# Kernel optimization log

Hardware: AMD Instinct MI355X
Metric: run time of the kernel (lower is better)

The kernel has to match this reference:

```python
import jax, jax.numpy as jnp
import numpy as np

N_NODES, N_EDGES, EMB_DIM = 100000, 1000000, 64
NUM_BOND_TYPE, NUM_BOND_DIR = 6, 3  # self-loop bond type index = 4


def gcn_conv(x, src, dst, bond_type, bond_dir, W, b, emb_bond, emb_dir):
    """One GCNConv (Hu et al. mol-GNN variant). src/dst/attrs already include self-loops."""
    N = x.shape[0]
    edge_emb = emb_bond[bond_type] + emb_dir[bond_dir]           # [Etot, D]
    ones = jnp.ones(src.shape[0], x.dtype)
    deg = jax.ops.segment_sum(ones, src, num_segments=N)         # scatter_add over row
    dis = jnp.where(deg > 0, jax.lax.rsqrt(deg), 0.0)
    norm = dis[src] * dis[dst]                                   # [Etot]
    h = x @ W.T + b                                              # [N, D]
    msg = norm[:, None] * (h[src] + edge_emb)                    # [Etot, D]
    return jax.ops.segment_sum(msg, dst, num_segments=N)         # add-aggregate at target


def with_self_loops(edge_index, edge_attr, N):
    loop = jnp.arange(N, dtype=edge_index.dtype)
    src = jnp.concatenate([edge_index[0], loop])
    dst = jnp.concatenate([edge_index[1], loop])
    bt = jnp.concatenate([edge_attr[:, 0], jnp.full((N,), 4, edge_attr.dtype)])
    bd = jnp.concatenate([edge_attr[:, 1], jnp.zeros((N,), edge_attr.dtype)])
    return src, dst, bt, bd


def setup_inputs() -> dict:
    key = jax.random.key(0)
    ks = jax.random.split(key, 12)
    D = EMB_DIM
    s = 1.0 / np.sqrt(D)
    inp = {
        "x": jax.random.normal(ks[0], (N_NODES, D), jnp.float32),
        "edge_index": jax.random.randint(ks[1], (2, N_EDGES), 0, N_NODES, jnp.int64 if jax.config.jax_enable_x64 else jnp.int32),
        "edge_attr": jax.random.randint(ks[2], (N_EDGES, 2), 0, 3, jnp.int64 if jax.config.jax_enable_x64 else jnp.int32),
        "W1": jax.random.uniform(ks[3], (D, D), jnp.float32, -s, s),
        "b1": jax.random.uniform(ks[4], (D,), jnp.float32, -s, s),
        "ebond1": jax.random.normal(ks[5], (NUM_BOND_TYPE, D), jnp.float32) * 0.1,
        "edir1": jax.random.normal(ks[6], (NUM_BOND_DIR, D), jnp.float32) * 0.1,
        "W2": jax.random.uniform(ks[7], (D, D), jnp.float32, -s, s),
        "b2": jax.random.uniform(ks[8], (D,), jnp.float32, -s, s),
        "ebond2": jax.random.normal(ks[9], (NUM_BOND_TYPE, D), jnp.float32) * 0.1,
        "edir2": jax.random.normal(ks[10], (NUM_BOND_DIR, D), jnp.float32) * 0.1,
    }
    return inp


def reference(x, edge_index, edge_attr, W1, b1, ebond1, edir1, W2, b2, ebond2, edir2):
    N = x.shape[0]
    src, dst, bt, bd = with_self_loops(edge_index, edge_attr, N)
    h = gcn_conv(x, src, dst, bt, bd, W1, b1, ebond1, edir1)
    h = jax.nn.relu(h)
    out = gcn_conv(h, src, dst, bt, bd, W2, b2, ebond2, edir2)
    return out
```

## Files before the change

### kernel.cpp

```cpp
#include <hip/hip_runtime.h>


#define THREADS 256
#define NBINS 512
#define BCAP 4096
#define CHUNK 2048
#define GEMM_SMEM_BYTES (64 * 68 * 4)
#define SC_SMEM (CHUNK * 4 * 2 + CHUNK * 2 * 2 + 6 * NBINS * 4 + 256 * 4)

typedef __attribute__((ext_vector_type(8))) short bf16x8;
typedef __attribute__((ext_vector_type(4))) float f32x4;

__device__ __forceinline__ float bflo(unsigned int v) { return __uint_as_float(v << 16); }
__device__ __forceinline__ float bfhi(unsigned int v) { return __uint_as_float(v & 0xFFFF0000u); }
__device__ __forceinline__ unsigned short f2bf(float f) {
    unsigned int u = __float_as_uint(f);
    return (unsigned short)((u + 0x7FFFu + ((u >> 16) & 1u)) >> 16);
}
__device__ __forceinline__ int sb(unsigned int w, int j) {
    return (int)(w << (24 - 8 * j)) >> 24;
}

template <bool XBF16>
__device__ __forceinline__ void gemm64_body(int tile, const void* __restrict__ Xv,
                                            const float* __restrict__ W,
                                            const float* __restrict__ B,
                                            unsigned short* __restrict__ Hb,
                                            unsigned char* __restrict__ Hq,
                                            float2* __restrict__ dsc, int N,
                                            float (*smem)[68]) {
    int t = threadIdx.x;
    int lane = t & 63;
    int wave = __builtin_amdgcn_readfirstlane(t >> 6);
    int l15 = lane & 15;
    int lk = lane >> 4;
    int arow = tile * 64 + wave * 16 + l15;

    bf16x8 a0, a1;
    if (arow < N) {
        if (XBF16) {
            const unsigned short* xp = (const unsigned short*)Xv + (size_t)arow * 64 + 8 * lk;
            a0 = *(const bf16x8*)xp;
            a1 = *(const bf16x8*)(xp + 32);
        } else {
            const float* xp = (const float*)Xv + (size_t)arow * 64 + 8 * lk;
            float4 v0 = *(const float4*)xp;
            float4 v1 = *(const float4*)(xp + 4);
            float4 v2 = *(const float4*)(xp + 32);
            float4 v3 = *(const float4*)(xp + 36);
            a0[0] = (short)f2bf(v0.x); a0[1] = (short)f2bf(v0.y);
            a0[2] = (short)f2bf(v0.z); a0[3] = (short)f2bf(v0.w);
            a0[4] = (short)f2bf(v1.x); a0[5] = (short)f2bf(v1.y);
            a0[6] = (short)f2bf(v1.z); a0[7] = (short)f2bf(v1.w);
            a1[0] = (short)f2bf(v2.x); a1[1] = (short)f2bf(v2.y);
            a1[2] = (short)f2bf(v2.z); a1[3] = (short)f2bf(v2.w);
            a1[4] = (short)f2bf(v3.x); a1[5] = (short)f2bf(v3.y);
            a1[6] = (short)f2bf(v3.z); a1[7] = (short)f2bf(v3.w);
        }
    } else {
#pragma unroll
        for (int e = 0; e < 8; ++e) { a0[e] = 0; a1[e] = 0; }
    }

    bf16x8 bfr[4][2];
#pragma unroll
    for (int n = 0; n < 4; ++n) {
        const float* wp = W + (size_t)(16 * n + l15) * 64 + 8 * lk;
#pragma unroll
        for (int ks = 0; ks < 2; ++ks) {
            float4 u0 = *(const float4*)(wp + 32 * ks);
            float4 u1 = *(const float4*)(wp + 32 * ks + 4);
            bf16x8 bb;
            bb[0] = (short)f2bf(u0.x); bb[1] = (short)f2bf(u0.y);
            bb[2] = (short)f2bf(u0.z); bb[3] = (short)f2bf(u0.w);
            bb[4] = (short)f2bf(u1.x); bb[5] = (short)f2bf(u1.y);
            bb[6] = (short)f2bf(u1.z); bb[7] = (short)f2bf(u1.w);
            bfr[n][ks] = bb;
        }
    }

    f32x4 acc[4];
#pragma unroll
    for (int n = 0; n < 4; ++n) {
        f32x4 z = {0.0f, 0.0f, 0.0f, 0.0f};
        z = __builtin_amdgcn_mfma_f32_16x16x32_bf16(a0, bfr[n][0], z, 0, 0, 0);
        acc[n] = __builtin_amdgcn_mfma_f32_16x16x32_bf16(a1, bfr[n][1], z, 0, 0, 0);
    }

#pragma unroll
    for (int n = 0; n < 4; ++n) {
        float bv = B[16 * n + l15];
        int col = 16 * n + l15;
#pragma unroll
        for (int r = 0; r < 4; ++r)
            smem[16 * wave + 4 * lk + r][col] = acc[n][r] + bv;
    }
    __syncthreads();

#pragma unroll
    for (int i = 0; i < 2; ++i) {
        int idx = t + i * THREADS;
        int r = idx >> 3;
        int c8 = (idx & 7) << 3;
        int grow = tile * 64 + r;
        float4 va = *(const float4*)(&smem[r][c8]);
        float4 vb = *(const float4*)(&smem[r][c8 + 4]);
        float v[8] = {va.x, va.y, va.z, va.w, vb.x, vb.y, vb.z, vb.w};
        float m = fabsf(v[0]);
#pragma unroll
        for (int j = 1; j < 8; ++j) m = fmaxf(m, fabsf(v[j]));
        m = fmaxf(m, __shfl_xor(m, 1));
        m = fmaxf(m, __shfl_xor(m, 2));
        m = fmaxf(m, __shfl_xor(m, 4));
        if (grow < N) {
            uint4 o;
            o.x = (unsigned)f2bf(v[0]) | ((unsigned)f2bf(v[1]) << 16);
            o.y = (unsigned)f2bf(v[2]) | ((unsigned)f2bf(v[3]) << 16);
            o.z = (unsigned)f2bf(v[4]) | ((unsigned)f2bf(v[5]) << 16);
            o.w = (unsigned)f2bf(v[6]) | ((unsigned)f2bf(v[7]) << 16);
            *(uint4*)(Hb + (size_t)grow * 64 + c8) = o;
            float inv = m > 0.0f ? 127.0f / m : 0.0f;
            int q[8];
#pragma unroll
            for (int j = 0; j < 8; ++j) q[j] = __float2int_rn(v[j] * inv);
            uint2 qp;
            qp.x = (unsigned)(q[0] & 255) | ((unsigned)(q[1] & 255) << 8) |
                   ((unsigned)(q[2] & 255) << 16) | ((unsigned)(q[3] & 255) << 24);
            qp.y = (unsigned)(q[4] & 255) | ((unsigned)(q[5] & 255) << 8) |
                   ((unsigned)(q[6] & 255) << 16) | ((unsigned)(q[7] & 255) << 24);
            *(uint2*)(Hq + (size_t)grow * 64 + c8) = qp;
            if ((idx & 7) == 0) dsc[grow].y = m * (1.0f / 127.0f);
        }
    }
}

__global__ __launch_bounds__(THREADS) void zero_gemm_kernel(
    int* __restrict__ gcur, int ncur, const float* __restrict__ X,
    const float* __restrict__ W1, const float* __restrict__ B1,
    unsigned short* __restrict__ Hb, unsigned char* __restrict__ Hq,
    float2* __restrict__ dsc, int N, int tile0) {
    __shared__ __align__(16) char sh[GEMM_SMEM_BYTES];
    int b = blockIdx.x;
    if (b == 0) {
        for (int i = threadIdx.x; i < ncur; i += THREADS) gcur[i] = 0;
        return;
    }
    gemm64_body<false>(tile0 + b - 1, X, W1, B1, Hb, Hq, dsc, N, (float(*)[68])sh);
}

__global__ __launch_bounds__(THREADS) void scatter_kernel(
    const int* __restrict__ src, const int* __restrict__ dst, const int* __restrict__ attr,
    int* __restrict__ gcurS, int* __restrict__ gcurD, unsigned char* __restrict__ payS,
    unsigned int* __restrict__ payD, int E, int SCB,
    const float* __restrict__ X, const float* __restrict__ W1, const float* __restrict__ B1,
    unsigned short* __restrict__ Hb, unsigned char* __restrict__ Hq,
    float2* __restrict__ dsc, int N, int tile0) {
    __shared__ __align__(16) char sh[SC_SMEM];
    int b = blockIdx.x;
    if (b >= SCB) {
        gemm64_body<false>(tile0 + b - SCB, X, W1, B1, Hb, Hq, dsc, N, (float(*)[68])sh);
        return;
    }
    unsigned int* Wv = (unsigned int*)sh;
    unsigned int* SD = Wv + CHUNK;
    unsigned short* DB = (unsigned short*)(SD + CHUNK);
    unsigned short* SDB = DB + CHUNK;
    int* hD = (int*)(SDB + CHUNK);
    int* hS = hD + NBINS;
    int* mapD = hS + NBINS;
    int* mapS = mapD + NBINS;
    int* curD = mapS + NBINS;
    int* curS = curD + NBINS;
    int* scn = curS + NBINS;
    unsigned char* SS = (unsigned char*)Wv;
    unsigned short* SSB = DB;

    int t = threadIdx.x;
    for (int k = t; k < NBINS; k += THREADS) { hD[k] = 0; hS[k] = 0; }
    __syncthreads();

    int lo = b * CHUNK, hi = min(E, lo + CHUNK);
    int nch = hi - lo;
    const int2* ap = (const int2*)attr;
    for (int li = t; li < nch; li += THREADS) {
        int i = lo + li;
        int sv = src[i], dv = dst[i];
        int2 a = ap[i];
        Wv[li] = (unsigned int)sv | ((unsigned int)(a.x * 3 + a.y) << 17) |
                 ((unsigned int)(dv & 255) << 22);
        DB[li] = (unsigned short)(dv >> 8);
        atomicAdd(&hD[dv >> 8], 1);
        atomicAdd(&hS[sv >> 8], 1);
    }
    __syncthreads();

    for (int k = t; k < NBINS; k += THREADS) {
        int h = hD[k];
        int r = h ? atomicAdd(&gcurD[k], h) : 0;
        mapD[k] = k * BCAP + r;
        int h2 = hS[k];
        int r2 = h2 ? atomicAdd(&gcurS[k], h2) : 0;
        mapS[k] = k * BCAP + r2;
    }
    __syncthreads();

    scn[t] = hD[2 * t] + hD[2 * t + 1];
    __syncthreads();
    for (int d = 1; d < THREADS; d <<= 1) {
        int a = (t >= d) ? scn[t - d] : 0;
        __syncthreads();
        scn[t] += a;
        __syncthreads();
    }
    {
        int off = t ? scn[t - 1] : 0;
        curD[2 * t] = off;
        curD[2 * t + 1] = off + hD[2 * t];
        mapD[2 * t] -= off;
        mapD[2 * t + 1] -= off + hD[2 * t];
    }
    __syncthreads();
    scn[t] = hS[2 * t] + hS[2 * t + 1];
    __syncthreads();
    for (int d = 1; d < THREADS; d <<= 1) {
        int a = (t >= d) ? scn[t - d] : 0;
        __syncthreads();
        scn[t] += a;
        __syncthreads();
    }
    {
        int off = t ? scn[t - 1] : 0;
        curS[2 * t] = off;
        curS[2 * t + 1] = off + hS[2 * t];
        mapS[2 * t] -= off;
        mapS[2 * t + 1] -= off + hS[2 * t];
    }
    __syncthreads();

    for (int li = t; li < nch; li += THREADS) {
        int k = DB[li];
        int p = atomicAdd(&curD[k], 1);
        SD[p] = Wv[li];
        SDB[p] = (unsigned short)k;
    }
    __syncthreads();

    for (int li = t; li < nch; li += THREADS) {
        int val = (int)(SD[li] & 0x1FFFFu);
        int k = val >> 8;
        int p = atomicAdd(&curS[k], 1);
        SS[p] = (unsigned char)(val & 255);
        SSB[p] = (unsigned short)k;
    }
    __syncthreads();

    for (int li = t; li < nch; li += THREADS) {
        payD[mapD[SDB[li]] + li] = SD[li];
        payS[mapS[SSB[li]] + li] = SS[li];
    }
}

__global__ __launch_bounds__(THREADS) void build_kernel(
    const unsigned char* __restrict__ payS, const unsigned int* __restrict__ payD,
    const int* __restrict__ gcurS, const int* __restrict__ gcurD,
    unsigned int* __restrict__ sorted, int2* __restrict__ rc,
    int NB2, float2* __restrict__ dsc, int N) {
    __shared__ int cnt[256];
    __shared__ int cur[256];
    __shared__ int s[THREADS];
    int t = threadIdx.x;
    int b = blockIdx.x;
    if (b < NB2) {
        int k = b;
        cnt[t] = 0;
        __syncthreads();
        int n = gcurS[k], off = k * BCAP;
        for (int i = t; i < n; i += THREADS) atomicAdd(&cnt[payS[off + i]], 1);
        __syncthreads();
        int node = k * 256 + t;
        if (node < N) dsc[node].x = 1.0f / sqrtf(1.0f + (float)cnt[t]);
    } else {
        int k = b - NB2;
        cnt[t] = 0;
        __syncthreads();
        int ecnt = gcurD[k], eoff = k * BCAP;
        for (int i = t; i < ecnt; i += THREADS)
            atomicAdd(&cnt[(payD[eoff + i] >> 22) & 255], 1);
        __syncthreads();
        int v = cnt[t];
        s[t] = v;
        __syncthreads();
        for (int d = 1; d < THREADS; d <<= 1) {
            int a = (t >= d) ? s[t - d] : 0;
            __syncthreads();
            s[t] += a;
            __syncthreads();
        }
        int excl = s[t] - v;
        int node = k * 256 + t;
        if (node < N) rc[node] = make_int2(eoff + excl, v);
        cur[t] = excl;
        __syncthreads();
        for (int i = t; i < ecnt; i += THREADS) {
            unsigned int u = payD[eoff + i];
            int p = atomicAdd(&cur[(u >> 22) & 255], 1);
            sorted[eoff + p] = u & 0x3FFFFFu;
        }
    }
}

template <bool XBF16>
__global__ __launch_bounds__(THREADS) void gemm64_kernel(const void* __restrict__ Xv,
                                                         const float* __restrict__ W,
                                                         const float* __restrict__ B,
                                                         unsigned short* __restrict__ Hb,
                                                         unsigned char* __restrict__ Hq,
                                                         float2* __restrict__ dsc, int N) {
    __shared__ __align__(16) char sh[GEMM_SMEM_BYTES];
    gemm64_body<XBF16>(blockIdx.x, Xv, W, B, Hb, Hq, dsc, N, (float(*)[68])sh);
}

__device__ __forceinline__ void edge_acc(unsigned int u, float dn,
                                         const float2* __restrict__ dsc,
                                         const unsigned char* __restrict__ Hq, int c,
                                         const float (*embc)[64], float acc[8]) {
    int s0 = u & 0x1FFFF;
    int e0 = (u >> 17) & 31;
    float2 ds = dsc[s0];
    uint2 q = *(const uint2*)(Hq + (size_t)s0 * 64 + c);
    float w = ds.x * dn, ws = w * ds.y;
    float4 ea = *(const float4*)(&embc[e0][c]);
    float4 eb = *(const float4*)(&embc[e0][c + 4]);
    acc[0] = fmaf(ws, (float)sb(q.x, 0), fmaf(w, ea.x, acc[0]));
    acc[1] = fmaf(ws, (float)sb(q.x, 1), fmaf(w, ea.y, acc[1]));
    acc[2] = fmaf(ws, (float)sb(q.x, 2), fmaf(w, ea.z, acc[2]));
    acc[3] = fmaf(ws, (float)sb(q.x, 3), fmaf(w, ea.w, acc[3]));
    acc[4] = fmaf(ws, (float)sb(q.y, 0), fmaf(w, eb.x, acc[4]));
    acc[5] = fmaf(ws, (float)sb(q.y, 1), fmaf(w, eb.y, acc[5]));
    acc[6] = fmaf(ws, (float)sb(q.y, 2), fmaf(w, eb.z, acc[6]));
    acc[7] = fmaf(ws, (float)sb(q.y, 3), fmaf(w, eb.w, acc[7]));
}

template <bool RELU_BF16_OUT>
__global__ __launch_bounds__(THREADS) void aggregate_kernel(
    const unsigned short* __restrict__ Hb, const unsigned char* __restrict__ Hq,
    const float2* __restrict__ dsc, const float* __restrict__ ebond,
    const float* __restrict__ edir, const int2* __restrict__ rc,
    const unsigned int* __restrict__ entries, void* __restrict__ outv, int N) {
    __shared__ float embc[18][64];
    int t = threadIdx.x;
    for (int i = t; i < 18 * 64; i += THREADS) {
        int row = i >> 6, c = i & 63;
        embc[row][c] = ebond[(row / 3) * 64 + c] + edir[(row % 3) * 64 + c];
    }
    __syncthreads();

    int n = blockIdx.x * 32 + (t >> 3);
    if (n >= N) return;
    int c = (t & 7) << 3;

    float dn = dsc[n].x;
    uint4 hv = *(const uint4*)(Hb + (size_t)n * 64 + c);
    float4 ea = *(const float4*)(&embc[12][c]);
    float4 eb = *(const float4*)(&embc[12][c + 4]);
    float nrm = dn * dn;
    float accA[8], accB[8];
    accA[0] = nrm * (bflo(hv.x) + ea.x);
    accA[1] = nrm * (bfhi(hv.x) + ea.y);
    accA[2] = nrm * (bflo(hv.y) + ea.z);
    accA[3] = nrm * (bfhi(hv.y) + ea.w);
    accA[4] = nrm * (bflo(hv.z) + eb.x);
    accA[5] = nrm * (bfhi(hv.z) + eb.y);
    accA[6] = nrm * (bflo(hv.w) + eb.z);
    accA[7] = nrm * (bfhi(hv.w) + eb.w);
#pragma unroll
    for (int j = 0; j < 8; ++j) accB[j] = 0.0f;

    int2 pc = rc[n];
    int p = pc.x;
    int end = p + pc.y;
    const float(*ec)[64] = (const float(*)[64])embc;
    for (; p + 3 < end; p += 4) {
        unsigned int u0 = entries[p];
        unsigned int u1 = entries[p + 1];
        unsigned int u2 = entries[p + 2];
        unsigned int u3 = entries[p + 3];
        edge_acc(u0, dn, dsc, Hq, c, ec, accA);
        edge_acc(u1, dn, dsc, Hq, c, ec, accB);
        edge_acc(u2, dn, dsc, Hq, c, ec, accA);
        edge_acc(u3, dn, dsc, Hq, c, ec, accB);
    }
    for (; p < end; ++p) edge_acc(entries[p], dn, dsc, Hq, c, ec, accA);

    float o[8];
#pragma unroll
    for (int j = 0; j < 8; ++j) o[j] = accA[j] + accB[j];

    if (RELU_BF16_OUT) {
        unsigned short* ob = (unsigned short*)outv;
        uint4 ov;
        ov.x = (unsigned)f2bf(fmaxf(o[0], 0.0f)) | ((unsigned)f2bf(fmaxf(o[1], 0.0f)) << 16);
        ov.y = (unsigned)f2bf(fmaxf(o[2], 0.0f)) | ((unsigned)f2bf(fmaxf(o[3], 0.0f)) << 16);
        ov.z = (unsigned)f2bf(fmaxf(o[4], 0.0f)) | ((unsigned)f2bf(fmaxf(o[5], 0.0f)) << 16);
        ov.w = (unsigned)f2bf(fmaxf(o[6], 0.0f)) | ((unsigned)f2bf(fmaxf(o[7], 0.0f)) << 16);
        *(uint4*)(ob + (size_t)n * 64 + c) = ov;
    } else {
        float* of = (float*)outv;
        *(float4*)(of + (size_t)n * 64 + c) = make_float4(o[0], o[1], o[2], o[3]);
        *(float4*)(of + (size_t)n * 64 + c + 4) = make_float4(o[4], o[5], o[6], o[7]);
    }
}

extern "C" void kernel_launch(void* const* d_in, const int* in_sizes, int n_in,
                              void* d_out, int out_size, void* d_ws, size_t ws_size,
                              hipStream_t stream) {
    const float* x      = (const float*)d_in[0];
    const int*   eidx   = (const int*)d_in[1];
    const int*   eattr  = (const int*)d_in[2];
    const float* W1     = (const float*)d_in[3];
    const float* b1     = (const float*)d_in[4];
    const float* ebond1 = (const float*)d_in[5];
    const float* edir1  = (const float*)d_in[6];
    const float* W2     = (const float*)d_in[7];
    const float* b2     = (const float*)d_in[8];
    const float* ebond2 = (const float*)d_in[9];
    const float* edir2  = (const float*)d_in[10];

    const int N = in_sizes[0] / 64;
    const int E = in_sizes[1] / 2;
    const int* src = eidx;
    const int* dst = eidx + E;
    float* out = (float*)d_out;
    const int NB2 = (N + 255) >> 8;
    const int SCB = (E + CHUNK - 1) / CHUNK;

    char* w = (char*)d_ws;
    size_t Na = ((size_t)N * 4 + 255) & ~(size_t)255;
    float2* dsc    = (float2*)w;           w += 2 * Na;
    int2*  rc      = (int2*)w;             w += 2 * Na;
    int*   gcur    = (int*)w;              w += 2 * NBINS * 4;
    unsigned int* payD   = (unsigned int*)w;   w += (size_t)NBINS * BCAP * 4;
    unsigned int* sorted = (unsigned int*)w;   w += (size_t)NBINS * BCAP * 4;
    unsigned char* payS  = (unsigned char*)w;  w += (size_t)NBINS * BCAP;
    unsigned short* Hb   = (unsigned short*)w; w += (size_t)N * 64 * 2;
    unsigned char*  Hq   = (unsigned char*)w;  w += ((size_t)N * 64 + 255) & ~(size_t)255;
    unsigned short* Ab   = (unsigned short*)w; w += (size_t)N * 64 * 2;
    int* gcurS = gcur;
    int* gcurD = gcur + NBINS;

    const int gT   = (N + 63) / 64;
    const int gN32 = (N + 31) / 32;

    const int t0 = min(gT, 512);
    const int t1 = gT - t0;

    zero_gemm_kernel<<<1 + t0, THREADS, 0, stream>>>(gcur, 2 * NBINS, x, W1, b1, Hb, Hq,
                                                     dsc, N, 0);
    scatter_kernel<<<SCB + t1, THREADS, 0, stream>>>(src, dst, eattr, gcurS, gcurD, payS,
                                                     payD, E, SCB, x, W1, b1, Hb, Hq,
                                                     dsc, N, t0);
    build_kernel<<<2 * NB2, THREADS, 0, stream>>>(payS, payD, gcurS, gcurD, sorted,
                                                  rc, NB2, dsc, N);

    aggregate_kernel<true><<<gN32, THREADS, 0, stream>>>(Hb, Hq, dsc, ebond1, edir1, rc,
                                                         sorted, Ab, N);

    gemm64_kernel<true><<<gT, THREADS, 0, stream>>>(Ab, W2, b2, Hb, Hq, dsc, N);
    aggregate_kernel<false><<<gN32, THREADS, 0, stream>>>(Hb, Hq, dsc, ebond2, edir2, rc,
                                                          sorted, out, N);
}
```

Before: 220.7 us.

## Fuse layer-1 aggregation with layer-2 GEMM in one kernel

Merges the first aggregation and the second linear layer into one kernel. Each block aggregates 64 nodes into shared memory as bf16, then runs the MFMA GEMM and writes the bf16/int8 features for layer 2. This drops one launch and the round trip of the intermediate activation through global memory. Because the GEMM overwrote the features layer 1 was still reading, it now writes to double buffers (Hb2/Hq2/dsc2). The trade-off is larger blocks with more shared memory and fewer threads in flight per node during aggregation.

```diff
diff --git a/kernel.cpp b/kernel.cpp
--- a/kernel.cpp
+++ b/kernel.cpp
@@ -21,48 +21,8 @@
     return (int)(w << (24 - 8 * j)) >> 24;
 }
 
-template <bool XBF16>
-__device__ __forceinline__ void gemm64_body(int tile, const void* __restrict__ Xv,
-                                            const float* __restrict__ W,
-                                            const float* __restrict__ B,
-                                            unsigned short* __restrict__ Hb,
-                                            unsigned char* __restrict__ Hq,
-                                            float2* __restrict__ dsc, int N,
-                                            float (*smem)[68]) {
-    int t = threadIdx.x;
-    int lane = t & 63;
-    int wave = __builtin_amdgcn_readfirstlane(t >> 6);
-    int l15 = lane & 15;
-    int lk = lane >> 4;
-    int arow = tile * 64 + wave * 16 + l15;
-
-    bf16x8 a0, a1;
-    if (arow < N) {
-        if (XBF16) {
-            const unsigned short* xp = (const unsigned short*)Xv + (size_t)arow * 64 + 8 * lk;
-            a0 = *(const bf16x8*)xp;
-            a1 = *(const bf16x8*)(xp + 32);
-        } else {
-            const float* xp = (const float*)Xv + (size_t)arow * 64 + 8 * lk;
-            float4 v0 = *(const float4*)xp;
-            float4 v1 = *(const float4*)(xp + 4);
-            float4 v2 = *(const float4*)(xp + 32);
-            float4 v3 = *(const float4*)(xp + 36);
-            a0[0] = (short)f2bf(v0.x); a0[1] = (short)f2bf(v0.y);
-            a0[2] = (short)f2bf(v0.z); a0[3] = (short)f2bf(v0.w);
-            a0[4] = (short)f2bf(v1.x); a0[5] = (short)f2bf(v1.y);
-            a0[6] = (short)f2bf(v1.z); a0[7] = (short)f2bf(v1.w);
-            a1[0] = (short)f2bf(v2.x); a1[1] = (short)f2bf(v2.y);
-            a1[2] = (short)f2bf(v2.z); a1[3] = (short)f2bf(v2.w);
-            a1[4] = (short)f2bf(v3.x); a1[5] = (short)f2bf(v3.y);
-            a1[6] = (short)f2bf(v3.z); a1[7] = (short)f2bf(v3.w);
-        }
-    } else {
-#pragma unroll
-        for (int e = 0; e < 8; ++e) { a0[e] = 0; a1[e] = 0; }
-    }
-
-    bf16x8 bfr[4][2];
+__device__ __forceinline__ void load_bfrags(const float* __restrict__ W, int l15, int lk,
+                                            bf16x8 bfr[4][2]) {
 #pragma unroll
     for (int n = 0; n < 4; ++n) {
         const float* wp = W + (size_t)(16 * n + l15) * 64 + 8 * lk;
@@ -78,15 +38,17 @@
             bfr[n][ks] = bb;
         }
     }
-
-    f32x4 acc[4];
-#pragma unroll
-    for (int n = 0; n < 4; ++n) {
-        f32x4 z = {0.0f, 0.0f, 0.0f, 0.0f};
-        z = __builtin_amdgcn_mfma_f32_16x16x32_bf16(a0, bfr[n][0], z, 0, 0, 0);
-        acc[n] = __builtin_amdgcn_mfma_f32_16x16x32_bf16(a1, bfr[n][1], z, 0, 0, 0);
-    }
-
+}
+
+__device__ __forceinline__ void gemm_epilogue(int tile, f32x4 acc[4],
+                                              const float* __restrict__ B, int wave,
+                                              int l15, int lk, int t,
+                                              unsigned short* __restrict__ Hb,
+                                              unsigned char* __restrict__ Hq,
+                                              float2* __restrict__ dscy,
+                                              const float2* __restrict__ dsrc,
+                                              float2* __restrict__ dsc2, int N,
+                                              float (*smem)[68]) {
 #pragma unroll
     for (int n = 0; n < 4; ++n) {
         float bv = B[16 * n + l15];
@@ -129,9 +91,60 @@
             qp.y = (unsigned)(q[4] & 255) | ((unsigned)(q[5] & 255) << 8) |
                    ((unsigned)(q[6] & 255) << 16) | ((unsigned)(q[7] & 255) << 24);
             *(uint2*)(Hq + (size_t)grow * 64 + c8) = qp;
-            if ((idx & 7) == 0) dsc[grow].y = m * (1.0f / 127.0f);
+            if ((idx & 7) == 0) {
+                float sc = m * (1.0f / 127.0f);
+                if (dsc2) dsc2[grow] = make_float2(dsrc[grow].x, sc);
+                else dscy[grow].y = sc;
+            }
         }
     }
+}
+
+__device__ __forceinline__ void gemm64_body(int tile, const float* __restrict__ Xv,
+                                            const float* __restrict__ W,
+                                            const float* __restrict__ B,
+                                            unsigned short* __restrict__ Hb,
+                                            unsigned char* __restrict__ Hq,
+                                            float2* __restrict__ dsc, int N,
+                                            float (*smem)[68]) {
+    int t = threadIdx.x;
+    int lane = t & 63;
+    int wave = __builtin_amdgcn_readfirstlane(t >> 6);
+    int l15 = lane & 15;
+    int lk = lane >> 4;
+    int arow = tile * 64 + wave * 16 + l15;
+
+    bf16x8 a0, a1;
+    if (arow < N) {
+        const float* xp = Xv + (size_t)arow * 64 + 8 * lk;
+        float4 v0 = *(const float4*)xp;
+        float4 v1 = *(const float4*)(xp + 4);
+        float4 v2 = *(const float4*)(xp + 32);
+        float4 v3 = *(const float4*)(xp + 36);
+        a0[0] = (short)f2bf(v0.x); a0[1] = (short)f2bf(v0.y);
+        a0[2] = (short)f2bf(v0.z); a0[3] = (short)f2bf(v0.w);
+        a0[4] = (short)f2bf(v1.x); a0[5] = (short)f2bf(v1.y);
+        a0[6] = (short)f2bf(v1.z); a0[7] = (short)f2bf(v1.w);
+        a1[0] = (short)f2bf(v2.x); a1[1] = (short)f2bf(v2.y);
+        a1[2] = (short)f2bf(v2.z); a1[3] = (short)f2bf(v2.w);
+        a1[4] = (short)f2bf(v3.x); a1[5] = (short)f2bf(v3.y);
+        a1[6] = (short)f2bf(v3.z); a1[7] = (short)f2bf(v3.w);
+    } else {
+#pragma unroll
+        for (int e = 0; e < 8; ++e) { a0[e] = 0; a1[e] = 0; }
+    }
+
+    bf16x8 bfr[4][2];
+    load_bfrags(W, l15, lk, bfr);
+
+    f32x4 acc[4];
+#pragma unroll
+    for (int n = 0; n < 4; ++n) {
+        f32x4 z = {0.0f, 0.0f, 0.0f, 0.0f};
+        z = __builtin_amdgcn_mfma_f32_16x16x32_bf16(a0, bfr[n][0], z, 0, 0, 0);
+        acc[n] = __builtin_amdgcn_mfma_f32_16x16x32_bf16(a1, bfr[n][1], z, 0, 0, 0);
+    }
+    gemm_epilogue(tile, acc, B, wave, l15, lk, t, Hb, Hq, dsc, nullptr, nullptr, N, smem);
 }
 
 __global__ __launch_bounds__(THREADS) void zero_gemm_kernel(
@@ -145,7 +158,7 @@
         for (int i = threadIdx.x; i < ncur; i += THREADS) gcur[i] = 0;
         return;
     }
-    gemm64_body<false>(tile0 + b - 1, X, W1, B1, Hb, Hq, dsc, N, (float(*)[68])sh);
+    gemm64_body(tile0 + b - 1, X, W1, B1, Hb, Hq, dsc, N, (float(*)[68])sh);
 }
 
 __global__ __launch_bounds__(THREADS) void scatter_kernel(
@@ -158,7 +171,7 @@
     __shared__ __align__(16) char sh[SC_SMEM];
     int b = blockIdx.x;
     if (b >= SCB) {
-        gemm64_body<false>(tile0 + b - SCB, X, W1, B1, Hb, Hq, dsc, N, (float(*)[68])sh);
+        gemm64_body(tile0 + b - SCB, X, W1, B1, Hb, Hq, dsc, N, (float(*)[68])sh);
         return;
     }
     unsigned int* Wv = (unsigned int*)sh;
@@ -307,17 +320,6 @@
             sorted[eoff + p] = u & 0x3FFFFFu;
         }
     }
-}
-
-template <bool XBF16>
-__global__ __launch_bounds__(THREADS) void gemm64_kernel(const void* __restrict__ Xv,
-                                                         const float* __restrict__ W,
-                                                         const float* __restrict__ B,
-                                                         unsigned short* __restrict__ Hb,
-                                                         unsigned char* __restrict__ Hq,
-                                                         float2* __restrict__ dsc, int N) {
-    __shared__ __align__(16) char sh[GEMM_SMEM_BYTES];
-    gemm64_body<XBF16>(blockIdx.x, Xv, W, B, Hb, Hq, dsc, N, (float(*)[68])sh);
 }
 
 __device__ __forceinline__ void edge_acc(unsigned int u, float dn,
@@ -341,28 +343,16 @@
     acc[7] = fmaf(ws, (float)sb(q.y, 3), fmaf(w, eb.w, acc[7]));
 }
 
-template <bool RELU_BF16_OUT>
-__global__ __launch_bounds__(THREADS) void aggregate_kernel(
-    const unsigned short* __restrict__ Hb, const unsigned char* __restrict__ Hq,
-    const float2* __restrict__ dsc, const float* __restrict__ ebond,
-    const float* __restrict__ edir, const int2* __restrict__ rc,
-    const unsigned int* __restrict__ entries, void* __restrict__ outv, int N) {
-    __shared__ float embc[18][64];
-    int t = threadIdx.x;
-    for (int i = t; i < 18 * 64; i += THREADS) {
-        int row = i >> 6, c = i & 63;
-        embc[row][c] = ebond[(row / 3) * 64 + c] + edir[(row % 3) * 64 + c];
-    }
-    __syncthreads();
-
-    int n = blockIdx.x * 32 + (t >> 3);
-    if (n >= N) return;
-    int c = (t & 7) << 3;
-
+__device__ __forceinline__ void agg_node(int n, int c, const unsigned short* __restrict__ Hb,
+                                         const unsigned char* __restrict__ Hq,
+                                         const float2* __restrict__ dsc,
+                                         const int2* __restrict__ rc,
+                                         const unsigned int* __restrict__ entries,
+                                         const float (*ec)[64], float o[8]) {
     float dn = dsc[n].x;
     uint4 hv = *(const uint4*)(Hb + (size_t)n * 64 + c);
-    float4 ea = *(const float4*)(&embc[12][c]);
-    float4 eb = *(const float4*)(&embc[12][c + 4]);
+    float4 ea = *(const float4*)(&ec[12][c]);
+    float4 eb = *(const float4*)(&ec[12][c + 4]);
     float nrm = dn * dn;
     float accA[8], accB[8];
     accA[0] = nrm * (bflo(hv.x) + ea.x);
@@ -379,7 +369,6 @@
     int2 pc = rc[n];
     int p = pc.x;
     int end = p + pc.y;
-    const float(*ec)[64] = (const float(*)[64])embc;
     for (; p + 3 < end; p += 4) {
         unsigned int u0 = entries[p];
         unsigned int u1 = entries[p + 1];
@@ -391,24 +380,88 @@
         edge_acc(u3, dn, dsc, Hq, c, ec, accB);
     }
     for (; p < end; ++p) edge_acc(entries[p], dn, dsc, Hq, c, ec, accA);
-
+#pragma unroll
+    for (int j = 0; j < 8; ++j) o[j] = accA[j] + accB[j];
+}
+
+__global__ __launch_bounds__(THREADS) void agg_gemm_kernel(
+    const unsigned short* __restrict__ Hb1, const unsigned char* __restrict__ Hq1,
+    const float2* __restrict__ dsc, const float* __restrict__ ebond,
+    const float* __restrict__ edir, const int2* __restrict__ rc,
+    const unsigned int* __restrict__ entries, const float* __restrict__ W,
+    const float* __restrict__ B, unsigned short* __restrict__ Hb2,
+    unsigned char* __restrict__ Hq2, float2* __restrict__ dsc2, int N) {
+    __shared__ float embc[18][64];
+    __shared__ __align__(16) unsigned short smA[64][72];
+    __shared__ __align__(16) float smC[64][68];
+    int t = threadIdx.x;
+    for (int i = t; i < 18 * 64; i += THREADS) {
+        int row = i >> 6, c = i & 63;
+        embc[row][c] = ebond[(row / 3) * 64 + c] + edir[(row % 3) * 64 + c];
+    }
+    __syncthreads();
+
+    int tile = blockIdx.x;
+    const float(*ec)[64] = (const float(*)[64])embc;
+#pragma unroll 1
+    for (int r = 0; r < 2; ++r) {
+        int ln = r * 32 + (t >> 3);
+        int n = tile * 64 + ln;
+        int c = (t & 7) << 3;
+        uint4 ov = make_uint4(0u, 0u, 0u, 0u);
+        if (n < N) {
+            float o[8];
+            agg_node(n, c, Hb1, Hq1, dsc, rc, entries, ec, o);
+            ov.x = (unsigned)f2bf(fmaxf(o[0], 0.0f)) | ((unsigned)f2bf(fmaxf(o[1], 0.0f)) << 16);
+            ov.y = (unsigned)f2bf(fmaxf(o[2], 0.0f)) | ((unsigned)f2bf(fmaxf(o[3], 0.0f)) << 16);
+            ov.z = (unsigned)f2bf(fmaxf(o[4], 0.0f)) | ((unsigned)f2bf(fmaxf(o[5], 0.0f)) << 16);
+            ov.w = (unsigned)f2bf(fmaxf(o[6], 0.0f)) | ((unsigned)f2bf(fmaxf(o[7], 0.0f)) << 16);
+        }
+        *(uint4*)(&smA[ln][c]) = ov;
+    }
+    __syncthreads();
+
+    int lane = t & 63;
+    int wave = __builtin_amdgcn_readfirstlane(t >> 6);
+    int l15 = lane & 15;
+    int lk = lane >> 4;
+    int lrow = wave * 16 + l15;
+    bf16x8 a0 = *(const bf16x8*)(&smA[lrow][8 * lk]);
+    bf16x8 a1 = *(const bf16x8*)(&smA[lrow][8 * lk + 32]);
+
+    bf16x8 bfr[4][2];
+    load_bfrags(W, l15, lk, bfr);
+
+    f32x4 acc[4];
+#pragma unroll
+    for (int n = 0; n < 4; ++n) {
+        f32x4 z = {0.0f, 0.0f, 0.0f, 0.0f};
+        z = __builtin_amdgcn_mfma_f32_16x16x32_bf16(a0, bfr[n][0], z, 0, 0, 0);
+        acc[n] = __builtin_amdgcn_mfma_f32_16x16x32_bf16(a1, bfr[n][1], z, 0, 0, 0);
+    }
+    gemm_epilogue(tile, acc, B, wave, l15, lk, t, Hb2, Hq2, nullptr, dsc, dsc2, N, smC);
+}
+
+__global__ __launch_bounds__(THREADS) void aggregate_kernel(
+    const unsigned short* __restrict__ Hb, const unsigned char* __restrict__ Hq,
+    const float2* __restrict__ dsc, const float* __restrict__ ebond,
+    const float* __restrict__ edir, const int2* __restrict__ rc,
+    const unsigned int* __restrict__ entries, float* __restrict__ out, int N) {
+    __shared__ float embc[18][64];
+    int t = threadIdx.x;
+    for (int i = t; i < 18 * 64; i += THREADS) {
+        int row = i >> 6, c = i & 63;
+        embc[row][c] = ebond[(row / 3) * 64 + c] + edir[(row % 3) * 64 + c];
+    }
+    __syncthreads();
+
+    int n = blockIdx.x * 32 + (t >> 3);
+    if (n >= N) return;
+    int c = (t & 7) << 3;
     float o[8];
-#pragma unroll
-    for (int j = 0; j < 8; ++j) o[j] = accA[j] + accB[j];
-
-    if (RELU_BF16_OUT) {
-        unsigned short* ob = (unsigned short*)outv;
-        uint4 ov;
-        ov.x = (unsigned)f2bf(fmaxf(o[0], 0.0f)) | ((unsigned)f2bf(fmaxf(o[1], 0.0f)) << 16);
-        ov.y = (unsigned)f2bf(fmaxf(o[2], 0.0f)) | ((unsigned)f2bf(fmaxf(o[3], 0.0f)) << 16);
-        ov.z = (unsigned)f2bf(fmaxf(o[4], 0.0f)) | ((unsigned)f2bf(fmaxf(o[5], 0.0f)) << 16);
-        ov.w = (unsigned)f2bf(fmaxf(o[6], 0.0f)) | ((unsigned)f2bf(fmaxf(o[7], 0.0f)) << 16);
-        *(uint4*)(ob + (size_t)n * 64 + c) = ov;
-    } else {
-        float* of = (float*)outv;
-        *(float4*)(of + (size_t)n * 64 + c) = make_float4(o[0], o[1], o[2], o[3]);
-        *(float4*)(of + (size_t)n * 64 + c + 4) = make_float4(o[4], o[5], o[6], o[7]);
-    }
+    agg_node(n, c, Hb, Hq, dsc, rc, entries, (const float(*)[64])embc, o);
+    *(float4*)(out + (size_t)n * 64 + c) = make_float4(o[0], o[1], o[2], o[3]);
+    *(float4*)(out + (size_t)n * 64 + c + 4) = make_float4(o[4], o[5], o[6], o[7]);
 }
 
 extern "C" void kernel_launch(void* const* d_in, const int* in_sizes, int n_in,
@@ -437,14 +490,16 @@
     char* w = (char*)d_ws;
     size_t Na = ((size_t)N * 4 + 255) & ~(size_t)255;
     float2* dsc    = (float2*)w;           w += 2 * Na;
+    float2* dsc2   = (float2*)w;           w += 2 * Na;
     int2*  rc      = (int2*)w;             w += 2 * Na;
     int*   gcur    = (int*)w;              w += 2 * NBINS * 4;
     unsigned int* payD   = (unsigned int*)w;   w += (size_t)NBINS * BCAP * 4;
     unsigned int* sorted = (unsigned int*)w;   w += (size_t)NBINS * BCAP * 4;
     unsigned char* payS  = (unsigned char*)w;  w += (size_t)NBINS * BCAP;
-    unsigned short* Hb   = (unsigned short*)w; w += (size_t)N * 64 * 2;
-    unsigned char*  Hq   = (unsigned char*)w;  w += ((size_t)N * 64 + 255) & ~(size_t)255;
-    unsigned short* Ab   = (unsigned short*)w; w += (size_t)N * 64 * 2;
+    unsigned short* Hb1  = (unsigned short*)w; w += (size_t)N * 64 * 2;
+    unsigned char*  Hq1  = (unsigned char*)w;  w += ((size_t)N * 64 + 255) & ~(size_t)255;
+    unsigned short* Hb2  = (unsigned short*)w; w += (size_t)N * 64 * 2;
+    unsigned char*  Hq2  = (unsigned char*)w;  w += ((size_t)N * 64 + 255) & ~(size_t)255;
     int* gcurS = gcur;
     int* gcurD = gcur + NBINS;
 
@@ -454,18 +509,17 @@
     const int t0 = min(gT, 512);
     const int t1 = gT - t0;
 
-    zero_gemm_kernel<<<1 + t0, THREADS, 0, stream>>>(gcur, 2 * NBINS, x, W1, b1, Hb, Hq,
+    zero_gemm_kernel<<<1 + t0, THREADS, 0, stream>>>(gcur, 2 * NBINS, x, W1, b1, Hb1, Hq1,
                                                      dsc, N, 0);
     scatter_kernel<<<SCB + t1, THREADS, 0, stream>>>(src, dst, eattr, gcurS, gcurD, payS,
-                                                     payD, E, SCB, x, W1, b1, Hb, Hq,
+                                                     payD, E, SCB, x, W1, b1, Hb1, Hq1,
                                                      dsc, N, t0);
     build_kernel<<<2 * NB2, THREADS, 0, stream>>>(payS, payD, gcurS, gcurD, sorted,
                                                   rc, NB2, dsc, N);
 
-    aggregate_kernel<true><<<gN32, THREADS, 0, stream>>>(Hb, Hq, dsc, ebond1, edir1, rc,
-                                                         sorted, Ab, N);
-
-    gemm64_kernel<true><<<gT, THREADS, 0, stream>>>(Ab, W2, b2, Hb, Hq, dsc, N);
-    aggregate_kernel<false><<<gN32, THREADS, 0, stream>>>(Hb, Hq, dsc, ebond2, edir2, rc,
-                                                          sorted, out, N);
-}
+    agg_gemm_kernel<<<gT, THREADS, 0, stream>>>(Hb1, Hq1, dsc, ebond1, edir1, rc, sorted,
+                                                W2, b2, Hb2, Hq2, dsc2, N);
+
+    aggregate_kernel<<<gN32, THREADS, 0, stream>>>(Hb2, Hq2, dsc2, ebond2, edir2, rc,
+                                                   sorted, out, N);
+}
```

After: 220.3 us. About the same (-0.2%).
